# Optimization experiments

Measured on AMD Instinct MI355X. Metric: run time of the kernel, lower is better.

Reference implementation:

```python
import jax, jax.numpy as jnp
import numpy as np

# TensorProductConvLayer (DiffDock-style): gather -> edge-MLP-weighted fully
# connected tensor product (lmax=1 irreps) -> scatter-mean.
# in/out irreps: ns x0e + nv x1o + nv x1e + ns x0o ; sh irreps: 1x0e + 1x1o
NS, NV = 16, 4
N_NODES, N_EDGES = 8000, 160000
EDGE_FEAT = 3 * NS                      # 48
IRREPS_DIM = 2 * NS + 6 * NV            # 56
# per-path weight block sizes (fully-connected 'uvw' paths, mul2 = 1):
# [A:0e*0e->0e, B:1o*1o->0e, A:0e*1o->1o, B:1o*0e->1o, C:1e*1o->1o,
#  B:1o*1o->1e, C:1e*0e->1e, D:0o*1o->1e, C:1e*1o->0o, D:0o*0e->0o]
PATH_SIZES = [NS*NS, NV*NS, NS*NV, NV*NV, NV*NV, NV*NV, NV*NV, NS*NV, NV*NS, NS*NS]
W_NUMEL = sum(PATH_SIZES)               # 832
# component-normalized CG factors: 1x1->0 uses delta/sqrt(3); 1x1->1 uses eps/sqrt(2)
INV_SQRT3 = float(1.0 / np.sqrt(3.0))
INV_SQRT2 = float(1.0 / np.sqrt(2.0))
# element path normalization: 1/sqrt(total fan-in mul per output irrep)
A_SCAL = float(1.0 / np.sqrt(NS + NV))      # 0e / 0o outputs
A_VEC = float(1.0 / np.sqrt(NS + 2 * NV))   # 1o / 1e outputs


def setup_inputs() -> dict:
    key = jax.random.key(0)
    ks = jax.random.split(key, 6)
    node_attr = jax.random.normal(ks[0], (N_NODES, IRREPS_DIM), jnp.float32)
    edge_index = jax.random.randint(ks[1], (2, N_EDGES), 0, N_NODES)
    edge_attr = jax.random.normal(ks[2], (N_EDGES, EDGE_FEAT), jnp.float32)
    edge_sh = jax.random.normal(ks[3], (N_EDGES, 4), jnp.float32)
    s = float(1.0 / np.sqrt(EDGE_FEAT))
    fc_w1 = jax.random.normal(ks[4], (EDGE_FEAT, EDGE_FEAT), jnp.float32) * s
    fc_b1 = jnp.zeros((EDGE_FEAT,), jnp.float32)
    fc_w2 = jax.random.normal(ks[5], (EDGE_FEAT, W_NUMEL), jnp.float32) * s
    fc_b2 = jnp.zeros((W_NUMEL,), jnp.float32)
    return dict(node_attr=node_attr, edge_attr=edge_attr, edge_sh=edge_sh,
                fc_w1=fc_w1, fc_b1=fc_b1, fc_w2=fc_w2, fc_b2=fc_b2,
                edge_index=edge_index)


def _split_weights(w):
    outs, off = [], 0
    for sz in PATH_SIZES:
        outs.append(w[:, off:off + sz])
        off += sz
    return outs


def _tp_conv(node_attr, edge_attr, edge_sh, fc_w1, fc_b1, fc_w2, fc_b2, src, dst):
    # edge MLP -> per-edge tensor-product weights [E, 832]
    h = jax.nn.relu(edge_attr @ fc_w1 + fc_b1)
    w = h @ fc_w2 + fc_b2
    wA0, wB0, wA1, wB1, wC1, wB1e, wC1e, wD1e, wC0o, wD0o = _split_weights(w)

    x = node_attr[dst]                         # gather [E, 56]
    x0e = x[:, :NS]
    x1o = x[:, NS:NS + 3 * NV].reshape(-1, NV, 3)
    x1e = x[:, NS + 3 * NV:NS + 6 * NV].reshape(-1, NV, 3)
    x0o = x[:, NS + 6 * NV:]
    s0 = edge_sh[:, 0]
    s1 = edge_sh[:, 1:4]

    # ---- 0e output [E, ns]
    o0e = jnp.einsum('eu,euv->ev', x0e, wA0.reshape(-1, NS, NS)) * s0[:, None]
    dot_b = jnp.einsum('eui,ei->eu', x1o, s1) * INV_SQRT3   # 1o x 1o -> 0e
    o0e = (o0e + jnp.einsum('eu,euv->ev', dot_b, wB0.reshape(-1, NV, NS))) * A_SCAL

    # ---- 1o output [E, nv, 3]
    o1o = jnp.einsum('eu,euv->ev', x0e, wA1.reshape(-1, NS, NV))[:, :, None] * s1[:, None, :]
    o1o = o1o + jnp.einsum('eui,euv->evi', x1o, wB1.reshape(-1, NV, NV)) * s0[:, None, None]
    cr_e = jnp.cross(x1e, s1[:, None, :]) * INV_SQRT2       # 1e x 1o -> 1o
    o1o = (o1o + jnp.einsum('eui,euv->evi', cr_e, wC1.reshape(-1, NV, NV))) * A_VEC

    # ---- 1e output [E, nv, 3]
    cr_o = jnp.cross(x1o, s1[:, None, :]) * INV_SQRT2       # 1o x 1o -> 1e
    o1e = jnp.einsum('eui,euv->evi', cr_o, wB1e.reshape(-1, NV, NV))
    o1e = o1e + jnp.einsum('eui,euv->evi', x1e, wC1e.reshape(-1, NV, NV)) * s0[:, None, None]
    o1e = (o1e + jnp.einsum('eu,euv->ev', x0o, wD1e.reshape(-1, NS, NV))[:, :, None] * s1[:, None, :]) * A_VEC

    # ---- 0o output [E, ns]
    dot_c = jnp.einsum('eui,ei->eu', x1e, s1) * INV_SQRT3   # 1e x 1o -> 0o
    o0o = jnp.einsum('eu,euv->ev', dot_c, wC0o.reshape(-1, NV, NS))
    o0o = (o0o + jnp.einsum('eu,euv->ev', x0o, wD0o.reshape(-1, NS, NS)) * s0[:, None]) * A_SCAL

    tp = jnp.concatenate([o0e, o1o.reshape(-1, 3 * NV), o1e.reshape(-1, 3 * NV), o0o], axis=-1)

    # scatter-mean over source nodes
    summed = jax.ops.segment_sum(tp, src, num_segments=N_NODES)
    counts = jax.ops.segment_sum(jnp.ones((tp.shape[0],), tp.dtype), src, num_segments=N_NODES)
    return summed / jnp.maximum(counts, 1.0)[:, None]


def reference(node_attr, edge_attr, edge_sh, fc_w1, fc_b1, fc_w2, fc_b2, edge_index):
    src, dst = edge_index[0], edge_index[1]
    return _tp_conv(node_attr, edge_attr, edge_sh, fc_w1, fc_b1, fc_w2, fc_b2, src, dst)
```

## Files before the change

### kernel.cpp

```cpp
#include <hip/hip_runtime.h>
#include <hip/hip_fp16.h>

#define IRR    56
#define EF     48
#define WN     832
#define NEDGE  160000
#define NNODE  8000
#define NT     512
#define TE2    64
#define NTASK  (NEDGE / TE2)
#define GRID   NTASK

#define INV_SQRT3 0.5773502691896258f
#define INV_SQRT2 0.7071067811865476f
#define A_SCAL    0.22360679774997896f
#define A_VEC     0.20412414523193154f

typedef __bf16 bf16x8 __attribute__((ext_vector_type(8)));
typedef float  f32x4  __attribute__((ext_vector_type(4)));
typedef unsigned short u16x8 __attribute__((ext_vector_type(8)));
typedef unsigned short u16x4 __attribute__((ext_vector_type(4)));

__device__ __forceinline__ unsigned short f2bf(float f) {
    unsigned int u = __builtin_bit_cast(unsigned int, f);
    u += 0x7FFFu + ((u >> 16) & 1u);
    return (unsigned short)(u >> 16);
}

__global__ void k_setup(const float* __restrict__ w1, const float* __restrict__ b1,
                        const float* __restrict__ w2, const float* __restrict__ b2,
                        unsigned short* __restrict__ W1T, unsigned short* __restrict__ W2L,
                        const int* __restrict__ edge_index, int* __restrict__ hist)
{
    int o = blockIdx.x * 256 + threadIdx.x;
    if (o < 64 * 832) {
        int k = o / 832;
        int n = o - k * 832;
        float v = (k < EF) ? w2[k * WN + n] : ((k == EF) ? b2[n] : 0.f);
        int i = n >> 4, mm = n & 15;
        int f = k >> 5, q = (k >> 3) & 3, j = k & 7;
        int o2 = (((i * 2 + f) * 64) + (q * 16 + mm)) * 8 + j;
        W2L[o2] = f2bf(v);
    }
    if (o < EF * EF) { int k = o / EF, n = o - k * EF; W1T[n * 64 + k] = f2bf(w1[o]); }
    if (o < EF * 16) { int n = o >> 4, kk = EF + (o & 15); W1T[n * 64 + kk] = (kk == EF) ? f2bf(b1[n]) : (unsigned short)0; }
    if (o < NEDGE) atomicAdd(&hist[edge_index[o]], 1);
}

__global__ __launch_bounds__(NT, 4) void tp_fused(
    const float* __restrict__ node_attr,
    const float* __restrict__ edge_attr,
    const float* __restrict__ edge_sh,
    const int*   __restrict__ edge_index,
    const int*   __restrict__ hist,
    const unsigned short* __restrict__ W1T,
    const unsigned short* __restrict__ W2L,
    float* __restrict__ out)
{
    __shared__ __align__(16) unsigned char UGH[TE2 * 56 * 4];
    __shared__ __align__(16) float sF0[TE2 * 61];
    __shared__ __align__(16) float sF1[TE2 * 61];
    __shared__ __align__(16) float sO[TE2 * IRR];
    __shared__ int   sSrc[TE2], sDst[TE2];
    __shared__ float sInv[TE2];

    float*          sG = (float*)UGH;
    unsigned short* sH = (unsigned short*)UGH;

    const int tid   = threadIdx.x;
    const int lane  = tid & 63;
    const int wv    = tid >> 6;
    const int half  = wv >> 2;
    const int wl    = wv & 3;
    const int m     = lane & 15;
    const int quad  = lane >> 4;
    const int em    = wl * 16 + m;
    const int e0    = blockIdx.x * TE2;

    if (tid < TE2)          sSrc[tid]       = edge_index[e0 + tid];
    else if (tid < 2 * TE2) sDst[tid - TE2] = edge_index[NEDGE + e0 + tid - TE2];
    __syncthreads();

    {
        const float* nrow = node_attr + (size_t)sDst[em] * IRR;
        float* g = sG + em * 56;
        if (half == 0) {
            *(float4*)(g + quad * 4)        = *(const float4*)(nrow + quad * 4);
            *(float4*)(g + (quad + 4) * 4)  = *(const float4*)(nrow + (quad + 4) * 4);
        } else {
            *(float4*)(g + (quad + 8) * 4)  = *(const float4*)(nrow + (quad + 8) * 4);
            if (quad < 2) { int c = 12 + quad; *(float4*)(g + c * 4) = *(const float4*)(nrow + c * 4); }
        }
    }
    if (tid >= 256 && tid < 256 + TE2) {
        int e = tid - 256;
        sInv[e] = 1.0f / fmaxf((float)hist[sSrc[e]], 1.0f);
    }

    float4 sh4 = *(const float4*)&edge_sh[(size_t)(e0 + em) * 4];
    const float s0 = sh4.x, sx = sh4.y, sy = sh4.z, sz = sh4.w;

    __syncthreads();

    {
        const float* x = sG + em * 56;
        const float c0S = s0 * A_SCAL;
        const float c0V = s0 * A_VEC;
        const float cD3 = INV_SQRT3 * A_SCAL;
        const float cC2 = INV_SQRT2 * A_VEC;
        if (half == 0) {
            float* F = sF0 + em * 61;
            #pragma unroll
            for (int t = 0; t < 4; t++) {
                int u = quad * 4 + t;
                float x0e = x[u];
                F[u]      = x0e * c0S;
                F[20 + u] = x0e * A_VEC;
            }
            {
                int u = quad;
                float a0 = x[16 + u*3], a1 = x[16 + u*3 + 1], a2 = x[16 + u*3 + 2];
                float b0 = x[28 + u*3], b1 = x[28 + u*3 + 1], b2 = x[28 + u*3 + 2];
                F[16 + u] = (a0*sx + a1*sy + a2*sz) * cD3;
                F[36 + u*3 + 0] = a0 * c0V;
                F[36 + u*3 + 1] = a1 * c0V;
                F[36 + u*3 + 2] = a2 * c0V;
                F[48 + u*3 + 0] = (b1*sz - b2*sy) * cC2;
                F[48 + u*3 + 1] = (b2*sx - b0*sz) * cC2;
                F[48 + u*3 + 2] = (b0*sy - b1*sx) * cC2;
            }
        } else {
            float* F = sF1 + em * 61;
            {
                int u = quad;
                float a0 = x[16 + u*3], a1 = x[16 + u*3 + 1], a2 = x[16 + u*3 + 2];
                float b0 = x[28 + u*3], b1 = x[28 + u*3 + 1], b2 = x[28 + u*3 + 2];
                F[u*3 + 0]      = (a1*sz - a2*sy) * cC2;
                F[u*3 + 1]      = (a2*sx - a0*sz) * cC2;
                F[u*3 + 2]      = (a0*sy - a1*sx) * cC2;
                F[12 + u*3 + 0] = b0 * c0V;
                F[12 + u*3 + 1] = b1 * c0V;
                F[12 + u*3 + 2] = b2 * c0V;
                F[40 + u]       = (b0*sx + b1*sy + b2*sz) * cD3;
            }
            #pragma unroll
            for (int t = 0; t < 4; t++) {
                int u = quad * 4 + t;
                float x0o = x[40 + u];
                F[24 + u] = x0o * A_VEC;
                F[44 + u] = x0o * c0S;
            }
        }
    }

    bf16x8 hb0, hb1;
    if (half == 0) {
        const float* arow = edge_attr + (size_t)(e0 + em) * EF;
        float av0[8], av1[8];
        {
            float4 p0 = *(const float4*)(arow + quad * 8);
            float4 p1 = *(const float4*)(arow + quad * 8 + 4);
            av0[0]=p0.x; av0[1]=p0.y; av0[2]=p0.z; av0[3]=p0.w;
            av0[4]=p1.x; av0[5]=p1.y; av0[6]=p1.z; av0[7]=p1.w;
        }
        if (quad < 2) {
            float4 p0 = *(const float4*)(arow + 32 + quad * 8);
            float4 p1 = *(const float4*)(arow + 32 + quad * 8 + 4);
            av1[0]=p0.x; av1[1]=p0.y; av1[2]=p0.z; av1[3]=p0.w;
            av1[4]=p1.x; av1[5]=p1.y; av1[6]=p1.z; av1[7]=p1.w;
        } else {
            #pragma unroll
            for (int j = 0; j < 8; j++) av1[j] = 0.f;
            if (quad == 2) av1[0] = 1.f;
        }
        u16x8 ub0, ub1;
        #pragma unroll
        for (int j = 0; j < 8; j++) { ub0[j] = f2bf(av0[j]); ub1[j] = f2bf(av1[j]); }
        hb0 = __builtin_bit_cast(bf16x8, ub0);
        hb1 = __builtin_bit_cast(bf16x8, ub1);
    }

    __syncthreads();

    if (half == 0) {
        #pragma unroll
        for (int nth = 0; nth < 3; nth++) {
            bf16x8 a0 = __builtin_bit_cast(bf16x8, *(const u16x8*)&W1T[(nth*16 + m)*64 + quad*8]);
            bf16x8 a1 = __builtin_bit_cast(bf16x8, *(const u16x8*)&W1T[(nth*16 + m)*64 + 32 + quad*8]);
            f32x4 c = {0.f, 0.f, 0.f, 0.f};
            c = __builtin_amdgcn_mfma_f32_16x16x32_bf16(a0, hb0, c, 0, 0, 0);
            c = __builtin_amdgcn_mfma_f32_16x16x32_bf16(a1, hb1, c, 0, 0, 0);
            u16x4 hp;
            #pragma unroll
            for (int r = 0; r < 4; r++) hp[r] = f2bf(fmaxf(c[r], 0.f));
            *(u16x4*)&sH[em * 72 + nth*16 + quad*4] = hp;
        }
        if (quad == 3) {
            u16x4 b = {0x3F80, 0, 0, 0}, z = {0, 0, 0, 0};
            *(u16x4*)&sH[em * 72 + 48] = b;
            *(u16x4*)&sH[em * 72 + 52] = z;
            *(u16x4*)&sH[em * 72 + 56] = z;
            *(u16x4*)&sH[em * 72 + 60] = z;
        }
    }
    __syncthreads();

    bf16x8 HB0 = __builtin_bit_cast(bf16x8, *(const u16x8*)&sH[em * 72 + quad*8]);
    bf16x8 HB1 = __builtin_bit_cast(bf16x8, *(const u16x8*)&sH[em * 72 + 32 + quad*8]);

    const unsigned short* Wt = W2L + (size_t)half * 26 * 1024;

    if (half == 0) {
        const float* Fp = sF0 + em * 61;
        float oe[4] = {0.f,0.f,0.f,0.f};
        float sA[4] = {0.f,0.f,0.f,0.f};
        float t1[12] = {0.f,0.f,0.f,0.f,0.f,0.f,0.f,0.f,0.f,0.f,0.f,0.f};
        #pragma unroll
        for (int i = 0; i < 26; i++) {
            u16x8 Af = *(const u16x8*)&Wt[i * 1024 + lane * 8];
            u16x8 Bf = *(const u16x8*)&Wt[i * 1024 + 512 + lane * 8];
            f32x4 c = {0.f,0.f,0.f,0.f};
            c = __builtin_amdgcn_mfma_f32_16x16x32_bf16(__builtin_bit_cast(bf16x8, Af), HB0, c, 0, 0, 0);
            c = __builtin_amdgcn_mfma_f32_16x16x32_bf16(__builtin_bit_cast(bf16x8, Bf), HB1, c, 0, 0, 0);
            if (i < 20) {
                float f = Fp[i];
                #pragma unroll
                for (int r = 0; r < 4; r++) oe[r] += f * c[r];
            } else if (i < 24) {
                float f = Fp[20 + (i - 20)*4 + quad];
                #pragma unroll
                for (int r = 0; r < 4; r++) sA[r] += f * c[r];
            } else {
                int u = (i - 24)*4 + quad;
                #pragma unroll
                for (int i3 = 0; i3 < 3; i3++) {
                    float f = Fp[36 + u*3 + i3];
                    #pragma unroll
                    for (int r = 0; r < 4; r++) t1[i3*4 + r] += f * c[r];
                }
            }
        }
        #pragma unroll
        for (int r = 0; r < 4; r++) {
            sA[r] += __shfl_xor(sA[r], 16, 64);  sA[r] += __shfl_xor(sA[r], 32, 64);
        }
        #pragma unroll
        for (int i = 0; i < 12; i++) {
            t1[i] += __shfl_xor(t1[i], 16, 64);  t1[i] += __shfl_xor(t1[i], 32, 64);
        }
        float4 v0; v0.x = oe[0]; v0.y = oe[1]; v0.z = oe[2]; v0.w = oe[3];
        *(float4*)&sO[em * IRR + quad*4] = v0;
        if (quad == 0) {
            #pragma unroll
            for (int r = 0; r < 4; r++) {
                sO[em * IRR + 16 + r*3 + 0] = sA[r] * sx + t1[0*4 + r];
                sO[em * IRR + 16 + r*3 + 1] = sA[r] * sy + t1[1*4 + r];
                sO[em * IRR + 16 + r*3 + 2] = sA[r] * sz + t1[2*4 + r];
            }
        }
    } else {
        const float* Fp = sF1 + em * 61;
        float sD[4] = {0.f,0.f,0.f,0.f};
        float t1[12] = {0.f,0.f,0.f,0.f,0.f,0.f,0.f,0.f,0.f,0.f,0.f,0.f};
        float oo[4] = {0.f,0.f,0.f,0.f};
        #pragma unroll
        for (int i = 0; i < 26; i++) {
            u16x8 Af = *(const u16x8*)&Wt[i * 1024 + lane * 8];
            u16x8 Bf = *(const u16x8*)&Wt[i * 1024 + 512 + lane * 8];
            f32x4 c = {0.f,0.f,0.f,0.f};
            c = __builtin_amdgcn_mfma_f32_16x16x32_bf16(__builtin_bit_cast(bf16x8, Af), HB0, c, 0, 0, 0);
            c = __builtin_amdgcn_mfma_f32_16x16x32_bf16(__builtin_bit_cast(bf16x8, Bf), HB1, c, 0, 0, 0);
            if (i < 2) {
                int j = i*4 + quad;
                #pragma unroll
                for (int i3 = 0; i3 < 3; i3++) {
                    float f = Fp[j*3 + i3];
                    #pragma unroll
                    for (int r = 0; r < 4; r++) t1[i3*4 + r] += f * c[r];
                }
            } else if (i < 6) {
                float f = Fp[24 + (i - 2)*4 + quad];
                #pragma unroll
                for (int r = 0; r < 4; r++) sD[r] += f * c[r];
            } else {
                float f = Fp[40 + (i - 6)];
                #pragma unroll
                for (int r = 0; r < 4; r++) oo[r] += f * c[r];
            }
        }
        #pragma unroll
        for (int r = 0; r < 4; r++) {
            sD[r] += __shfl_xor(sD[r], 16, 64);  sD[r] += __shfl_xor(sD[r], 32, 64);
        }
        #pragma unroll
        for (int i = 0; i < 12; i++) {
            t1[i] += __shfl_xor(t1[i], 16, 64);  t1[i] += __shfl_xor(t1[i], 32, 64);
        }
        float4 v1; v1.x = oo[0]; v1.y = oo[1]; v1.z = oo[2]; v1.w = oo[3];
        *(float4*)&sO[em * IRR + 28 + 12 + quad*4] = v1;
        if (quad == 0) {
            #pragma unroll
            for (int r = 0; r < 4; r++) {
                sO[em * IRR + 28 + r*3 + 0] = sD[r] * sx + t1[0*4 + r];
                sO[em * IRR + 28 + r*3 + 1] = sD[r] * sy + t1[1*4 + r];
                sO[em * IRR + 28 + r*3 + 2] = sD[r] * sz + t1[2*4 + r];
            }
        }
    }

    __syncthreads();

    #pragma unroll
    for (int it = 0; it < 7; it++) {
        int idx = it * NT + tid;
        int e = idx / IRR, ch = idx - e * IRR;
        unsafeAtomicAdd(&out[(size_t)sSrc[e] * IRR + ch], sO[e * IRR + ch] * sInv[e]);
    }
}

extern "C" void kernel_launch(void* const* d_in, const int* in_sizes, int n_in,
                              void* d_out, int out_size, void* d_ws, size_t ws_size,
                              hipStream_t stream) {
    const float* node_attr  = (const float*)d_in[0];
    const float* edge_attr  = (const float*)d_in[1];
    const float* edge_sh    = (const float*)d_in[2];
    const float* fc_w1      = (const float*)d_in[3];
    const float* fc_b1      = (const float*)d_in[4];
    const float* fc_w2      = (const float*)d_in[5];
    const float* fc_b2      = (const float*)d_in[6];
    const int*   edge_index = (const int*)d_in[7];

    int* hist = (int*)d_ws;
    unsigned short* W1T = (unsigned short*)(hist + NNODE);
    unsigned short* W2L = W1T + EF * 64;

    hipMemsetAsync(hist, 0, NNODE * sizeof(int), stream);
    hipMemsetAsync(d_out, 0, (size_t)out_size * sizeof(float), stream);

    k_setup<<<(NEDGE + 255) / 256, 256, 0, stream>>>(
        fc_w1, fc_b1, fc_w2, fc_b2, W1T, W2L, edge_index, hist);

    tp_fused<<<GRID, NT, 0, stream>>>(node_attr, edge_attr, edge_sh, edge_index,
                                      hist, W1T, W2L, (float*)d_out);
}
```

Before: 168.7 us.

## Make tp_fused persistent with register prefetch of next edge tile

Converts the one-block-per-64-edge-tile kernel into a persistent grid of 512 blocks that stride over tiles. Each block keeps the first-layer MLP weights in registers and prefetches the next tile's indices, node rows, edge attributes and sh into registers while the current tile runs its second-layer MFMA work. The aim is to hide gather latency and avoid per-block launch and weight-reload cost. In exchange it uses more registers, and the grid is fixed at 512 blocks, which may not fill the GPU as well as the original 2500 blocks.

```diff
diff --git a/kernel.cpp b/kernel.cpp
--- a/kernel.cpp
+++ b/kernel.cpp
@@ -9,7 +9,8 @@
 #define NT     512
 #define TE2    64
 #define NTASK  (NEDGE / TE2)
-#define GRID   NTASK
+#define GRID   512
+#define STRIDE 512
 
 #define INV_SQRT3 0.5773502691896258f
 #define INV_SQRT2 0.7071067811865476f
@@ -57,264 +58,287 @@
     const unsigned short* __restrict__ W2L,
     float* __restrict__ out)
 {
-    __shared__ __align__(16) unsigned char UGH[TE2 * 56 * 4];
+    __shared__ __align__(16) float sG[TE2 * 56];
+    __shared__ __align__(16) unsigned short sH[TE2 * 72];
     __shared__ __align__(16) float sF0[TE2 * 61];
     __shared__ __align__(16) float sF1[TE2 * 61];
     __shared__ __align__(16) float sO[TE2 * IRR];
-    __shared__ int   sSrc[TE2], sDst[TE2];
+    __shared__ int   sSrc[TE2];
     __shared__ float sInv[TE2];
-
-    float*          sG = (float*)UGH;
-    unsigned short* sH = (unsigned short*)UGH;
 
     const int tid   = threadIdx.x;
     const int lane  = tid & 63;
     const int wv    = tid >> 6;
     const int half  = wv >> 2;
-    const int wl    = wv & 3;
     const int m     = lane & 15;
     const int quad  = lane >> 4;
-    const int em    = wl * 16 + m;
-    const int e0    = blockIdx.x * TE2;
-
-    if (tid < TE2)          sSrc[tid]       = edge_index[e0 + tid];
-    else if (tid < 2 * TE2) sDst[tid - TE2] = edge_index[NEDGE + e0 + tid - TE2];
-    __syncthreads();
-
-    {
-        const float* nrow = node_attr + (size_t)sDst[em] * IRR;
-        float* g = sG + em * 56;
+    const int em    = (wv & 3) * 16 + m;
+
+    bf16x8 a00 = __builtin_bit_cast(bf16x8, *(const u16x8*)&W1T[( 0 + m) * 64 + quad * 8]);
+    bf16x8 a01 = __builtin_bit_cast(bf16x8, *(const u16x8*)&W1T[( 0 + m) * 64 + 32 + quad * 8]);
+    bf16x8 a10 = __builtin_bit_cast(bf16x8, *(const u16x8*)&W1T[(16 + m) * 64 + quad * 8]);
+    bf16x8 a11 = __builtin_bit_cast(bf16x8, *(const u16x8*)&W1T[(16 + m) * 64 + 32 + quad * 8]);
+    bf16x8 a20 = __builtin_bit_cast(bf16x8, *(const u16x8*)&W1T[(32 + m) * 64 + quad * 8]);
+    bf16x8 a21 = __builtin_bit_cast(bf16x8, *(const u16x8*)&W1T[(32 + m) * 64 + 32 + quad * 8]);
+
+    float4 pg0, pg1;
+    float4 pa0, pa1, pa2, pa3;
+    float4 psh;
+    int    psrc; float pinv;
+
+    auto PREFETCH = [&](int t) {
+        const int pe = t * TE2 + em;
+        psrc = edge_index[pe];
+        const int pdst = edge_index[NEDGE + pe];
+        psh  = *(const float4*)&edge_sh[(size_t)pe * 4];
+        pinv = 1.0f / fmaxf((float)hist[psrc], 1.0f);
+        const float* nrow = node_attr + (size_t)pdst * IRR;
         if (half == 0) {
-            *(float4*)(g + quad * 4)        = *(const float4*)(nrow + quad * 4);
-            *(float4*)(g + (quad + 4) * 4)  = *(const float4*)(nrow + (quad + 4) * 4);
+            pg0 = *(const float4*)(nrow + quad * 4);
+            pg1 = *(const float4*)(nrow + (quad + 4) * 4);
+            const float* arow = edge_attr + (size_t)pe * EF;
+            pa0 = *(const float4*)(arow + quad * 8);
+            pa1 = *(const float4*)(arow + quad * 8 + 4);
+            if (quad < 2) {
+                pa2 = *(const float4*)(arow + 32 + quad * 8);
+                pa3 = *(const float4*)(arow + 32 + quad * 8 + 4);
+            } else {
+                pa2 = float4{0.f, 0.f, 0.f, 0.f};
+                pa3 = float4{0.f, 0.f, 0.f, 0.f};
+            }
         } else {
-            *(float4*)(g + (quad + 8) * 4)  = *(const float4*)(nrow + (quad + 8) * 4);
-            if (quad < 2) { int c = 12 + quad; *(float4*)(g + c * 4) = *(const float4*)(nrow + c * 4); }
-        }
-    }
-    if (tid >= 256 && tid < 256 + TE2) {
-        int e = tid - 256;
-        sInv[e] = 1.0f / fmaxf((float)hist[sSrc[e]], 1.0f);
-    }
-
-    float4 sh4 = *(const float4*)&edge_sh[(size_t)(e0 + em) * 4];
-    const float s0 = sh4.x, sx = sh4.y, sy = sh4.z, sz = sh4.w;
-
-    __syncthreads();
-
-    {
-        const float* x = sG + em * 56;
-        const float c0S = s0 * A_SCAL;
-        const float c0V = s0 * A_VEC;
-        const float cD3 = INV_SQRT3 * A_SCAL;
-        const float cC2 = INV_SQRT2 * A_VEC;
+            pg0 = *(const float4*)(nrow + (quad + 8) * 4);
+            int c = (quad < 2) ? (12 + quad) : 13;
+            pg1 = *(const float4*)(nrow + c * 4);
+        }
+    };
+
+    PREFETCH(blockIdx.x);
+
+    for (int task = blockIdx.x; task < NTASK; task += STRIDE) {
+        __syncthreads();
+
+        const float s0 = psh.x, sx = psh.y, sy = psh.z, sz = psh.w;
+        {
+            float* g = sG + em * 56;
+            if (half == 0) {
+                *(float4*)(g + quad * 4)       = pg0;
+                *(float4*)(g + (quad + 4) * 4) = pg1;
+                if (quad == 0) { sSrc[em] = psrc; sInv[em] = pinv; }
+            } else {
+                *(float4*)(g + (quad + 8) * 4) = pg0;
+                if (quad < 2) *(float4*)(g + (12 + quad) * 4) = pg1;
+            }
+        }
+        bf16x8 hb0, hb1;
         if (half == 0) {
-            float* F = sF0 + em * 61;
-            #pragma unroll
-            for (int t = 0; t < 4; t++) {
-                int u = quad * 4 + t;
-                float x0e = x[u];
-                F[u]      = x0e * c0S;
-                F[20 + u] = x0e * A_VEC;
-            }
-            {
-                int u = quad;
-                float a0 = x[16 + u*3], a1 = x[16 + u*3 + 1], a2 = x[16 + u*3 + 2];
-                float b0 = x[28 + u*3], b1 = x[28 + u*3 + 1], b2 = x[28 + u*3 + 2];
-                F[16 + u] = (a0*sx + a1*sy + a2*sz) * cD3;
-                F[36 + u*3 + 0] = a0 * c0V;
-                F[36 + u*3 + 1] = a1 * c0V;
-                F[36 + u*3 + 2] = a2 * c0V;
-                F[48 + u*3 + 0] = (b1*sz - b2*sy) * cC2;
-                F[48 + u*3 + 1] = (b2*sx - b0*sz) * cC2;
-                F[48 + u*3 + 2] = (b0*sy - b1*sx) * cC2;
+            float av0[8] = {pa0.x,pa0.y,pa0.z,pa0.w, pa1.x,pa1.y,pa1.z,pa1.w};
+            float av1[8] = {pa2.x,pa2.y,pa2.z,pa2.w, pa3.x,pa3.y,pa3.z,pa3.w};
+            if (quad == 2) av1[0] = 1.f;
+            u16x8 ub0, ub1;
+            #pragma unroll
+            for (int j = 0; j < 8; j++) { ub0[j] = f2bf(av0[j]); ub1[j] = f2bf(av1[j]); }
+            hb0 = __builtin_bit_cast(bf16x8, ub0);
+            hb1 = __builtin_bit_cast(bf16x8, ub1);
+        }
+
+        __syncthreads();
+
+        {
+            const float* x = sG + em * 56;
+            const float c0S = s0 * A_SCAL;
+            const float c0V = s0 * A_VEC;
+            const float cD3 = INV_SQRT3 * A_SCAL;
+            const float cC2 = INV_SQRT2 * A_VEC;
+            if (half == 0) {
+                float* F = sF0 + em * 61;
+                #pragma unroll
+                for (int t = 0; t < 4; t++) {
+                    int u = quad * 4 + t;
+                    float x0e = x[u];
+                    F[u]      = x0e * c0S;
+                    F[20 + u] = x0e * A_VEC;
+                }
+                {
+                    int u = quad;
+                    float aa0 = x[16 + u*3], aa1 = x[16 + u*3 + 1], aa2 = x[16 + u*3 + 2];
+                    float bb0 = x[28 + u*3], bb1 = x[28 + u*3 + 1], bb2 = x[28 + u*3 + 2];
+                    F[16 + u] = (aa0*sx + aa1*sy + aa2*sz) * cD3;
+                    F[36 + u*3 + 0] = aa0 * c0V;
+                    F[36 + u*3 + 1] = aa1 * c0V;
+                    F[36 + u*3 + 2] = aa2 * c0V;
+                    F[48 + u*3 + 0] = (bb1*sz - bb2*sy) * cC2;
+                    F[48 + u*3 + 1] = (bb2*sx - bb0*sz) * cC2;
+                    F[48 + u*3 + 2] = (bb0*sy - bb1*sx) * cC2;
+                }
+            } else {
+                float* F = sF1 + em * 61;
+                {
+                    int u = quad;
+                    float aa0 = x[16 + u*3], aa1 = x[16 + u*3 + 1], aa2 = x[16 + u*3 + 2];
+                    float bb0 = x[28 + u*3], bb1 = x[28 + u*3 + 1], bb2 = x[28 + u*3 + 2];
+                    F[u*3 + 0]      = (aa1*sz - aa2*sy) * cC2;
+                    F[u*3 + 1]      = (aa2*sx - aa0*sz) * cC2;
+                    F[u*3 + 2]      = (aa0*sy - aa1*sx) * cC2;
+                    F[12 + u*3 + 0] = bb0 * c0V;
+                    F[12 + u*3 + 1] = bb1 * c0V;
+                    F[12 + u*3 + 2] = bb2 * c0V;
+                    F[40 + u]       = (bb0*sx + bb1*sy + bb2*sz) * cD3;
+                }
+                #pragma unroll
+                for (int t = 0; t < 4; t++) {
+                    int u = quad * 4 + t;
+                    float x0o = x[40 + u];
+                    F[24 + u] = x0o * A_VEC;
+                    F[44 + u] = x0o * c0S;
+                }
+            }
+        }
+
+        if (half == 0) {
+            f32x4 c0 = {0.f,0.f,0.f,0.f}, c1 = {0.f,0.f,0.f,0.f}, c2 = {0.f,0.f,0.f,0.f};
+            c0 = __builtin_amdgcn_mfma_f32_16x16x32_bf16(a00, hb0, c0, 0, 0, 0);
+            c0 = __builtin_amdgcn_mfma_f32_16x16x32_bf16(a01, hb1, c0, 0, 0, 0);
+            c1 = __builtin_amdgcn_mfma_f32_16x16x32_bf16(a10, hb0, c1, 0, 0, 0);
+            c1 = __builtin_amdgcn_mfma_f32_16x16x32_bf16(a11, hb1, c1, 0, 0, 0);
+            c2 = __builtin_amdgcn_mfma_f32_16x16x32_bf16(a20, hb0, c2, 0, 0, 0);
+            c2 = __builtin_amdgcn_mfma_f32_16x16x32_bf16(a21, hb1, c2, 0, 0, 0);
+            u16x4 h0, h1, h2;
+            #pragma unroll
+            for (int r = 0; r < 4; r++) {
+                h0[r] = f2bf(fmaxf(c0[r], 0.f));
+                h1[r] = f2bf(fmaxf(c1[r], 0.f));
+                h2[r] = f2bf(fmaxf(c2[r], 0.f));
+            }
+            *(u16x4*)&sH[em * 72 +  0 + quad*4] = h0;
+            *(u16x4*)&sH[em * 72 + 16 + quad*4] = h1;
+            *(u16x4*)&sH[em * 72 + 32 + quad*4] = h2;
+            if (quad == 3) {
+                u16x4 b = {0x3F80, 0, 0, 0}, z = {0, 0, 0, 0};
+                *(u16x4*)&sH[em * 72 + 48] = b;
+                *(u16x4*)&sH[em * 72 + 52] = z;
+                *(u16x4*)&sH[em * 72 + 56] = z;
+                *(u16x4*)&sH[em * 72 + 60] = z;
+            }
+        }
+        __syncthreads();
+
+        bf16x8 HB0 = __builtin_bit_cast(bf16x8, *(const u16x8*)&sH[em * 72 + quad*8]);
+        bf16x8 HB1 = __builtin_bit_cast(bf16x8, *(const u16x8*)&sH[em * 72 + 32 + quad*8]);
+
+        {
+            int nt_ = task + STRIDE;
+            PREFETCH(nt_ < NTASK ? nt_ : task);
+        }
+
+        const unsigned short* Wt = W2L + (size_t)half * 26 * 1024;
+
+        if (half == 0) {
+            const float* Fp = sF0 + em * 61;
+            float oe[4] = {0.f,0.f,0.f,0.f};
+            float sA[4] = {0.f,0.f,0.f,0.f};
+            float t1[12] = {0.f,0.f,0.f,0.f,0.f,0.f,0.f,0.f,0.f,0.f,0.f,0.f};
+            #pragma unroll
+            for (int i = 0; i < 26; i++) {
+                u16x8 Af = *(const u16x8*)&Wt[i * 1024 + lane * 8];
+                u16x8 Bf = *(const u16x8*)&Wt[i * 1024 + 512 + lane * 8];
+                f32x4 c = {0.f,0.f,0.f,0.f};
+                c = __builtin_amdgcn_mfma_f32_16x16x32_bf16(__builtin_bit_cast(bf16x8, Af), HB0, c, 0, 0, 0);
+                c = __builtin_amdgcn_mfma_f32_16x16x32_bf16(__builtin_bit_cast(bf16x8, Bf), HB1, c, 0, 0, 0);
+                if (i < 20) {
+                    float f = Fp[i];
+                    #pragma unroll
+                    for (int r = 0; r < 4; r++) oe[r] += f * c[r];
+                } else if (i < 24) {
+                    float f = Fp[20 + (i - 20)*4 + quad];
+                    #pragma unroll
+                    for (int r = 0; r < 4; r++) sA[r] += f * c[r];
+                } else {
+                    int u = (i - 24)*4 + quad;
+                    #pragma unroll
+                    for (int i3 = 0; i3 < 3; i3++) {
+                        float f = Fp[36 + u*3 + i3];
+                        #pragma unroll
+                        for (int r = 0; r < 4; r++) t1[i3*4 + r] += f * c[r];
+                    }
+                }
+            }
+            #pragma unroll
+            for (int r = 0; r < 4; r++) {
+                sA[r] += __shfl_xor(sA[r], 16, 64);  sA[r] += __shfl_xor(sA[r], 32, 64);
+            }
+            #pragma unroll
+            for (int i = 0; i < 12; i++) {
+                t1[i] += __shfl_xor(t1[i], 16, 64);  t1[i] += __shfl_xor(t1[i], 32, 64);
+            }
+            float4 v0; v0.x = oe[0]; v0.y = oe[1]; v0.z = oe[2]; v0.w = oe[3];
+            *(float4*)&sO[em * IRR + quad*4] = v0;
+            if (quad == 0) {
+                #pragma unroll
+                for (int r = 0; r < 4; r++) {
+                    sO[em * IRR + 16 + r*3 + 0] = sA[r] * sx + t1[0*4 + r];
+                    sO[em * IRR + 16 + r*3 + 1] = sA[r] * sy + t1[1*4 + r];
+                    sO[em * IRR + 16 + r*3 + 2] = sA[r] * sz + t1[2*4 + r];
+                }
             }
         } else {
-            float* F = sF1 + em * 61;
-            {
-                int u = quad;
-                float a0 = x[16 + u*3], a1 = x[16 + u*3 + 1], a2 = x[16 + u*3 + 2];
-                float b0 = x[28 + u*3], b1 = x[28 + u*3 + 1], b2 = x[28 + u*3 + 2];
-                F[u*3 + 0]      = (a1*sz - a2*sy) * cC2;
-                F[u*3 + 1]      = (a2*sx - a0*sz) * cC2;
-                F[u*3 + 2]      = (a0*sy - a1*sx) * cC2;
-                F[12 + u*3 + 0] = b0 * c0V;
-                F[12 + u*3 + 1] = b1 * c0V;
-                F[12 + u*3 + 2] = b2 * c0V;
-                F[40 + u]       = (b0*sx + b1*sy + b2*sz) * cD3;
-            }
-            #pragma unroll
-            for (int t = 0; t < 4; t++) {
-                int u = quad * 4 + t;
-                float x0o = x[40 + u];
-                F[24 + u] = x0o * A_VEC;
-                F[44 + u] = x0o * c0S;
-            }
-        }
-    }
-
-    bf16x8 hb0, hb1;
-    if (half == 0) {
-        const float* arow = edge_attr + (size_t)(e0 + em) * EF;
-        float av0[8], av1[8];
-        {
-            float4 p0 = *(const float4*)(arow + quad * 8);
-            float4 p1 = *(const float4*)(arow + quad * 8 + 4);
-            av0[0]=p0.x; av0[1]=p0.y; av0[2]=p0.z; av0[3]=p0.w;
-            av0[4]=p1.x; av0[5]=p1.y; av0[6]=p1.z; av0[7]=p1.w;
-        }
-        if (quad < 2) {
-            float4 p0 = *(const float4*)(arow + 32 + quad * 8);
-            float4 p1 = *(const float4*)(arow + 32 + quad * 8 + 4);
-            av1[0]=p0.x; av1[1]=p0.y; av1[2]=p0.z; av1[3]=p0.w;
-            av1[4]=p1.x; av1[5]=p1.y; av1[6]=p1.z; av1[7]=p1.w;
-        } else {
-            #pragma unroll
-            for (int j = 0; j < 8; j++) av1[j] = 0.f;
-            if (quad == 2) av1[0] = 1.f;
-        }
-        u16x8 ub0, ub1;
+            const float* Fp = sF1 + em * 61;
+            float sD[4] = {0.f,0.f,0.f,0.f};
+            float t1[12] = {0.f,0.f,0.f,0.f,0.f,0.f,0.f,0.f,0.f,0.f,0.f,0.f};
+            float oo[4] = {0.f,0.f,0.f,0.f};
+            #pragma unroll
+            for (int i = 0; i < 26; i++) {
+                u16x8 Af = *(const u16x8*)&Wt[i * 1024 + lane * 8];
+                u16x8 Bf = *(const u16x8*)&Wt[i * 1024 + 512 + lane * 8];
+                f32x4 c = {0.f,0.f,0.f,0.f};
+                c = __builtin_amdgcn_mfma_f32_16x16x32_bf16(__builtin_bit_cast(bf16x8, Af), HB0, c, 0, 0, 0);
+                c = __builtin_amdgcn_mfma_f32_16x16x32_bf16(__builtin_bit_cast(bf16x8, Bf), HB1, c, 0, 0, 0);
+                if (i < 2) {
+                    int j = i*4 + quad;
+                    #pragma unroll
+                    for (int i3 = 0; i3 < 3; i3++) {
+                        float f = Fp[j*3 + i3];
+                        #pragma unroll
+                        for (int r = 0; r < 4; r++) t1[i3*4 + r] += f * c[r];
+                    }
+                } else if (i < 6) {
+                    float f = Fp[24 + (i - 2)*4 + quad];
+                    #pragma unroll
+                    for (int r = 0; r < 4; r++) sD[r] += f * c[r];
+                } else {
+                    float f = Fp[40 + (i - 6)];
+                    #pragma unroll
+                    for (int r = 0; r < 4; r++) oo[r] += f * c[r];
+                }
+            }
+            #pragma unroll
+            for (int r = 0; r < 4; r++) {
+                sD[r] += __shfl_xor(sD[r], 16, 64);  sD[r] += __shfl_xor(sD[r], 32, 64);
+            }
+            #pragma unroll
+            for (int i = 0; i < 12; i++) {
+                t1[i] += __shfl_xor(t1[i], 16, 64);  t1[i] += __shfl_xor(t1[i], 32, 64);
+            }
+            float4 v1; v1.x = oo[0]; v1.y = oo[1]; v1.z = oo[2]; v1.w = oo[3];
+            *(float4*)&sO[em * IRR + 28 + 12 + quad*4] = v1;
+            if (quad == 0) {
+                #pragma unroll
+                for (int r = 0; r < 4; r++) {
+                    sO[em * IRR + 28 + r*3 + 0] = sD[r] * sx + t1[0*4 + r];
+                    sO[em * IRR + 28 + r*3 + 1] = sD[r] * sy + t1[1*4 + r];
+                    sO[em * IRR + 28 + r*3 + 2] = sD[r] * sz + t1[2*4 + r];
+                }
+            }
+        }
+
+        __syncthreads();
+
         #pragma unroll
-        for (int j = 0; j < 8; j++) { ub0[j] = f2bf(av0[j]); ub1[j] = f2bf(av1[j]); }
-        hb0 = __builtin_bit_cast(bf16x8, ub0);
-        hb1 = __builtin_bit_cast(bf16x8, ub1);
-    }
-
-    __syncthreads();
-
-    if (half == 0) {
-        #pragma unroll
-        for (int nth = 0; nth < 3; nth++) {
-            bf16x8 a0 = __builtin_bit_cast(bf16x8, *(const u16x8*)&W1T[(nth*16 + m)*64 + quad*8]);
-            bf16x8 a1 = __builtin_bit_cast(bf16x8, *(const u16x8*)&W1T[(nth*16 + m)*64 + 32 + quad*8]);
-            f32x4 c = {0.f, 0.f, 0.f, 0.f};
-            c = __builtin_amdgcn_mfma_f32_16x16x32_bf16(a0, hb0, c, 0, 0, 0);
-            c = __builtin_amdgcn_mfma_f32_16x16x32_bf16(a1, hb1, c, 0, 0, 0);
-            u16x4 hp;
-            #pragma unroll
-            for (int r = 0; r < 4; r++) hp[r] = f2bf(fmaxf(c[r], 0.f));
-            *(u16x4*)&sH[em * 72 + nth*16 + quad*4] = hp;
-        }
-        if (quad == 3) {
-            u16x4 b = {0x3F80, 0, 0, 0}, z = {0, 0, 0, 0};
-            *(u16x4*)&sH[em * 72 + 48] = b;
-            *(u16x4*)&sH[em * 72 + 52] = z;
-            *(u16x4*)&sH[em * 72 + 56] = z;
-            *(u16x4*)&sH[em * 72 + 60] = z;
-        }
-    }
-    __syncthreads();
-
-    bf16x8 HB0 = __builtin_bit_cast(bf16x8, *(const u16x8*)&sH[em * 72 + quad*8]);
-    bf16x8 HB1 = __builtin_bit_cast(bf16x8, *(const u16x8*)&sH[em * 72 + 32 + quad*8]);
-
-    const unsigned short* Wt = W2L + (size_t)half * 26 * 1024;
-
-    if (half == 0) {
-        const float* Fp = sF0 + em * 61;
-        float oe[4] = {0.f,0.f,0.f,0.f};
-        float sA[4] = {0.f,0.f,0.f,0.f};
-        float t1[12] = {0.f,0.f,0.f,0.f,0.f,0.f,0.f,0.f,0.f,0.f,0.f,0.f};
-        #pragma unroll
-        for (int i = 0; i < 26; i++) {
-            u16x8 Af = *(const u16x8*)&Wt[i * 1024 + lane * 8];
-            u16x8 Bf = *(const u16x8*)&Wt[i * 1024 + 512 + lane * 8];
-            f32x4 c = {0.f,0.f,0.f,0.f};
-            c = __builtin_amdgcn_mfma_f32_16x16x32_bf16(__builtin_bit_cast(bf16x8, Af), HB0, c, 0, 0, 0);
-            c = __builtin_amdgcn_mfma_f32_16x16x32_bf16(__builtin_bit_cast(bf16x8, Bf), HB1, c, 0, 0, 0);
-            if (i < 20) {
-                float f = Fp[i];
-                #pragma unroll
-                for (int r = 0; r < 4; r++) oe[r] += f * c[r];
-            } else if (i < 24) {
-                float f = Fp[20 + (i - 20)*4 + quad];
-                #pragma unroll
-                for (int r = 0; r < 4; r++) sA[r] += f * c[r];
-            } else {
-                int u = (i - 24)*4 + quad;
-                #pragma unroll
-                for (int i3 = 0; i3 < 3; i3++) {
-                    float f = Fp[36 + u*3 + i3];
-                    #pragma unroll
-                    for (int r = 0; r < 4; r++) t1[i3*4 + r] += f * c[r];
-                }
-            }
-        }
-        #pragma unroll
-        for (int r = 0; r < 4; r++) {
-            sA[r] += __shfl_xor(sA[r], 16, 64);  sA[r] += __shfl_xor(sA[r], 32, 64);
-        }
-        #pragma unroll
-        for (int i = 0; i < 12; i++) {
-            t1[i] += __shfl_xor(t1[i], 16, 64);  t1[i] += __shfl_xor(t1[i], 32, 64);
-        }
-        float4 v0; v0.x = oe[0]; v0.y = oe[1]; v0.z = oe[2]; v0.w = oe[3];
-        *(float4*)&sO[em * IRR + quad*4] = v0;
-        if (quad == 0) {
-            #pragma unroll
-            for (int r = 0; r < 4; r++) {
-                sO[em * IRR + 16 + r*3 + 0] = sA[r] * sx + t1[0*4 + r];
-                sO[em * IRR + 16 + r*3 + 1] = sA[r] * sy + t1[1*4 + r];
-                sO[em * IRR + 16 + r*3 + 2] = sA[r] * sz + t1[2*4 + r];
-            }
-        }
-    } else {
-        const float* Fp = sF1 + em * 61;
-        float sD[4] = {0.f,0.f,0.f,0.f};
-        float t1[12] = {0.f,0.f,0.f,0.f,0.f,0.f,0.f,0.f,0.f,0.f,0.f,0.f};
-        float oo[4] = {0.f,0.f,0.f,0.f};
-        #pragma unroll
-        for (int i = 0; i < 26; i++) {
-            u16x8 Af = *(const u16x8*)&Wt[i * 1024 + lane * 8];
-            u16x8 Bf = *(const u16x8*)&Wt[i * 1024 + 512 + lane * 8];
-            f32x4 c = {0.f,0.f,0.f,0.f};
-            c = __builtin_amdgcn_mfma_f32_16x16x32_bf16(__builtin_bit_cast(bf16x8, Af), HB0, c, 0, 0, 0);
-            c = __builtin_amdgcn_mfma_f32_16x16x32_bf16(__builtin_bit_cast(bf16x8, Bf), HB1, c, 0, 0, 0);
-            if (i < 2) {
-                int j = i*4 + quad;
-                #pragma unroll
-                for (int i3 = 0; i3 < 3; i3++) {
-                    float f = Fp[j*3 + i3];
-                    #pragma unroll
-                    for (int r = 0; r < 4; r++) t1[i3*4 + r] += f * c[r];
-                }
-            } else if (i < 6) {
-                float f = Fp[24 + (i - 2)*4 + quad];
-                #pragma unroll
-                for (int r = 0; r < 4; r++) sD[r] += f * c[r];
-            } else {
-                float f = Fp[40 + (i - 6)];
-                #pragma unroll
-                for (int r = 0; r < 4; r++) oo[r] += f * c[r];
-            }
-        }
-        #pragma unroll
-        for (int r = 0; r < 4; r++) {
-            sD[r] += __shfl_xor(sD[r], 16, 64);  sD[r] += __shfl_xor(sD[r], 32, 64);
-        }
-        #pragma unroll
-        for (int i = 0; i < 12; i++) {
-            t1[i] += __shfl_xor(t1[i], 16, 64);  t1[i] += __shfl_xor(t1[i], 32, 64);
-        }
-        float4 v1; v1.x = oo[0]; v1.y = oo[1]; v1.z = oo[2]; v1.w = oo[3];
-        *(float4*)&sO[em * IRR + 28 + 12 + quad*4] = v1;
-        if (quad == 0) {
-            #pragma unroll
-            for (int r = 0; r < 4; r++) {
-                sO[em * IRR + 28 + r*3 + 0] = sD[r] * sx + t1[0*4 + r];
-                sO[em * IRR + 28 + r*3 + 1] = sD[r] * sy + t1[1*4 + r];
-                sO[em * IRR + 28 + r*3 + 2] = sD[r] * sz + t1[2*4 + r];
-            }
-        }
-    }
-
-    __syncthreads();
-
-    #pragma unroll
-    for (int it = 0; it < 7; it++) {
-        int idx = it * NT + tid;
-        int e = idx / IRR, ch = idx - e * IRR;
-        unsafeAtomicAdd(&out[(size_t)sSrc[e] * IRR + ch], sO[e * IRR + ch] * sInv[e]);
+        for (int it = 0; it < 7; it++) {
+            int idx = it * NT + tid;
+            int e = idx / IRR, ch = idx - e * IRR;
+            unsafeAtomicAdd(&out[(size_t)sSrc[e] * IRR + ch], sO[e * IRR + ch] * sInv[e]);
+        }
     }
 }
 
```

Measured after the change: 267.8 us. 1.59x slower.
